# Performance work log

Hardware: AMD Instinct MI355X
Metric: run time of the kernel (lower is better)

The kernel has to match this reference:

```python
import jax, jax.numpy as jnp
import numpy as np

B, S, N, HID = 4, 512, 128, 64


def setup_inputs() -> dict:
    key = jax.random.key(0)
    ks = jax.random.split(key, 32)
    def rn(k, shape, scale=0.1):
        return jax.random.normal(k, shape, dtype=jnp.float32) * scale
    adj = jax.random.randint(ks[0], (N, N), 0, 2).astype(jnp.int32)
    adj = adj.at[jnp.arange(N), jnp.arange(N)].set(1)  # self loops
    inp = {
        'x': jax.random.normal(ks[1], (B, S, N, 1), dtype=jnp.float32),
        'adj': adj,
        'emb_w': rn(ks[2], (1, 16)), 'emb_b': jnp.zeros((16,), jnp.float32),
        'gat1_W': rn(ks[3], (16, 16)), 'gat1_a': rn(ks[4], (32, 1)),
        'gat2_W': rn(ks[5], (16, 8)), 'gat2_a': rn(ks[6], (16, 1)),
        'Wih0': rn(ks[7], (4 * HID, N)), 'Whh0': rn(ks[8], (4 * HID, HID)),
        'bih0': jnp.zeros((4 * HID,), jnp.float32), 'bhh0': jnp.zeros((4 * HID,), jnp.float32),
        'Wih1': rn(ks[9], (4 * HID, HID)), 'Whh1': rn(ks[10], (4 * HID, HID)),
        'bih1': jnp.zeros((4 * HID,), jnp.float32), 'bhh1': jnp.zeros((4 * HID,), jnp.float32),
    }
    comb = HID + 8 * N
    for i, name in enumerate(['dir', 'ret', 'vol']):
        o = 2 if name == 'vol' else 1
        inp[name + '_w1'] = rn(ks[11 + 4 * i], (comb, 32))
        inp[name + '_b1'] = jnp.zeros((32,), jnp.float32)
        inp[name + '_w2'] = rn(ks[12 + 4 * i], (32, o))
        inp[name + '_b2'] = jnp.zeros((o,), jnp.float32)
    return inp


def _gat(h, W, a, mask):
    # e_ij = leakyrelu(a1 . Wh_i + a2 . Wh_j): avoid torch's [M,N,N,2F] concat.
    Wh = h @ W                                  # [M, N, F]
    Fo = W.shape[1]
    f1 = Wh @ a[:Fo]                            # [M, N, 1]
    f2 = Wh @ a[Fo:]                            # [M, N, 1]
    e = jax.nn.leaky_relu(f1 + jnp.swapaxes(f2, 1, 2), 0.2)  # [M, N, N]
    e = jnp.where(mask, e, jnp.float32(-9e15))
    attn = jax.nn.softmax(e, axis=2)
    return attn @ Wh                            # [M, N, F]


def _lstm_layer(xs, Wih, Whh, bih, bhh):
    # xs: [S, B, I]; PyTorch gate order i, f, g, o
    Bsz = xs.shape[1]
    Hd = Whh.shape[1]
    def step(carry, xt):
        h, c = carry
        g = xt @ Wih.T + h @ Whh.T + bih + bhh
        i, f, gg, o = jnp.split(g, 4, axis=-1)
        c = jax.nn.sigmoid(f) * c + jax.nn.sigmoid(i) * jnp.tanh(gg)
        h = jax.nn.sigmoid(o) * jnp.tanh(c)
        return (h, c), h
    init = (jnp.zeros((Bsz, Hd), xs.dtype), jnp.zeros((Bsz, Hd), xs.dtype))
    _, hs = jax.lax.scan(step, init, xs)
    return hs


def reference(x, adj, emb_w, emb_b, gat1_W, gat1_a, gat2_W, gat2_a,
              Wih0, Whh0, bih0, bhh0, Wih1, Whh1, bih1, bhh1,
              dir_w1, dir_b1, dir_w2, dir_b2,
              ret_w1, ret_b1, ret_w2, ret_b2,
              vol_w1, vol_b1, vol_w2, vol_b2):
    Bz, Sz, Nz, _ = x.shape
    mask = (adj > 0)[None]                      # [1, N, N], broadcast over B*S
    xe = (x @ emb_w + emb_b).reshape(Bz * Sz, Nz, 16)
    xg = jax.nn.elu(_gat(xe, gat1_W, gat1_a, mask))   # gat1 concat=True -> elu
    xg = _gat(xg, gat2_W, gat2_a, mask)               # gat2 concat=False
    xg_out = xg.reshape(Bz, Sz, Nz * 8)[:, -1, :]
    xs = jnp.swapaxes(x.reshape(Bz, Sz, Nz), 0, 1)    # [S, B, N]
    hs = _lstm_layer(xs, Wih0, Whh0, bih0, bhh0)
    hs = _lstm_layer(hs, Wih1, Whh1, bih1, bhh1)      # inter-layer dropout off (eval)
    xl_out = hs[-1]                                   # [B, 64]
    c = jnp.concatenate([xl_out, xg_out], axis=1)     # [B, 64 + 8N]
    def head(w1, b1, w2, b2):
        return jax.nn.relu(c @ w1 + b1) @ w2 + b2
    return (head(dir_w1, dir_b1, dir_w2, dir_b2),
            head(ret_w1, ret_b1, ret_w2, ret_b2),
            head(vol_w1, vol_b1, vol_w2, vol_b2))
```

## Files before the change

kernel.cpp:

```cpp
#include <hip/hip_runtime.h>

#define SEQ   512
#define BATCH 4
#define NN    128
#define HID   64
#define G4    256
#define MAGIC 0x13579BDF

typedef _Float16 half2v __attribute__((ext_vector_type(2)));

__device__ __forceinline__ float frcp(float x)  { return __builtin_amdgcn_rcpf(x); }
__device__ __forceinline__ float fsigm(float x) { return frcp(1.f + __expf(-x)); }
__device__ __forceinline__ float ftanh(float x) { return 1.f - 2.f * frcp(1.f + __expf(2.f * x)); }
__device__ __forceinline__ float lrelu(float x) { return x > 0.f ? x : 0.2f * x; }
__device__ __forceinline__ float dot4f(float4 w, float4 h) {
  return fmaf(w.x, h.x, fmaf(w.y, h.y, fmaf(w.z, h.z, w.w * h.w)));
}
__device__ __forceinline__ void pin4(float4& v) {
  asm volatile("" : "+v"(v.x), "+v"(v.y), "+v"(v.z), "+v"(v.w));
}
__device__ __forceinline__ float qsum(float x) {
  x += __int_as_float(__builtin_amdgcn_update_dpp(
      0, __float_as_int(x), 0xB1, 0xF, 0xF, true));
  x += __int_as_float(__builtin_amdgcn_update_dpp(
      0, __float_as_int(x), 0x4E, 0xF, 0xF, true));
  return x;
}
__device__ __forceinline__ half2v u2h(unsigned u) {
  return __builtin_bit_cast(half2v, u);
}
__device__ __forceinline__ half2v pk16(float lo, float hi) {
  return __builtin_bit_cast(half2v, __builtin_amdgcn_cvt_pkrtz(lo, hi));
}
__device__ __forceinline__ float fdot2(half2v a, half2v b, float c) {
#if __has_builtin(__builtin_amdgcn_fdot2)
  return __builtin_amdgcn_fdot2(a, b, c, false);
#else
  float d = c;
  asm("v_dot2_f32_f16 %0, %1, %2, %0" : "+v"(d) : "v"(a), "v"(b));
  return d;
#endif
}
__device__ __forceinline__ float dot8h(const half2v* w, const uint4& a,
                                       const uint4& b, float acc) {
  acc = fdot2(w[0], u2h(a.x), acc);
  acc = fdot2(w[1], u2h(a.y), acc);
  acc = fdot2(w[2], u2h(a.z), acc);
  acc = fdot2(w[3], u2h(a.w), acc);
  acc = fdot2(w[4], u2h(b.x), acc);
  acc = fdot2(w[5], u2h(b.y), acc);
  acc = fdot2(w[6], u2h(b.z), acc);
  acc = fdot2(w[7], u2h(b.w), acc);
  return acc;
}

#define BAR_LDS() asm volatile("s_waitcnt lgkmcnt(0)\n\ts_barrier" ::: "memory")

__global__ __attribute__((amdgpu_flat_work_group_size(256, 256),
                          amdgpu_waves_per_eu(1, 4)))
void fused_all(
    const float* __restrict__ x, const int* __restrict__ adj,
    const float* __restrict__ emb_w, const float* __restrict__ emb_b,
    const float* __restrict__ W1, const float* __restrict__ a1,
    const float* __restrict__ W2, const float* __restrict__ a2,
    const float* __restrict__ Wih0, const float* __restrict__ Whh0,
    const float* __restrict__ bih0, const float* __restrict__ bhh0,
    const float* __restrict__ Wih1, const float* __restrict__ Whh1,
    const float* __restrict__ bih1, const float* __restrict__ bhh1,
    const float* __restrict__ dw1, const float* __restrict__ db1,
    const float* __restrict__ dw2, const float* __restrict__ db2,
    const float* __restrict__ rw1, const float* __restrict__ rb1,
    const float* __restrict__ rw2, const float* __restrict__ rb2,
    const float* __restrict__ vw1, const float* __restrict__ vb1,
    const float* __restrict__ vw2, const float* __restrict__ vb2,
    float* __restrict__ X0T, float* __restrict__ xg,
    int* __restrict__ flags, float* __restrict__ out)
{
  const int bid = blockIdx.x;
  const int tid = threadIdx.x;

  if (bid >= 4) {
    const int c = bid - 4;
    __shared__ __align__(16) float xls[NN];
    {
      const int g = tid;
      float4 w4[32];
      {
        const float4* wp = reinterpret_cast<const float4*>(Wih0 + g * NN);
#pragma unroll
        for (int i = 0; i < 32; ++i) w4[i] = wp[i];
#pragma unroll
        for (int i = 0; i < 32; ++i) pin4(w4[i]);
      }
      const float bsum = bih0[g] + bhh0[g];
      for (int phase = 0; phase < 4; ++phase) {
        const int T = c + 128 * phase;
        for (int bb = 0; bb < BATCH; ++bb) {
          if (tid < NN) xls[tid] = x[(bb * SEQ + T) * NN + tid];
          __syncthreads();
          {
            const float4* hp = reinterpret_cast<const float4*>(xls);
            float p0 = 0.f, p1 = 0.f, p2 = 0.f, p3 = 0.f;
#pragma unroll
            for (int k = 0; k < 32; k += 4) {
              p0 += dot4f(w4[k],     hp[k]);
              p1 += dot4f(w4[k + 1], hp[k + 1]);
              p2 += dot4f(w4[k + 2], hp[k + 2]);
              p3 += dot4f(w4[k + 3], hp[k + 3]);
            }
            X0T[(4 * T + bb) * G4 + (g & 63) * 4 + (g >> 6)] =
                ((p0 + p1) + (p2 + p3)) + bsum;
          }
          __syncthreads();
        }
        if (tid == 0 && phase == 0)
          __hip_atomic_store(&flags[c], MAGIC, __ATOMIC_RELEASE,
                             __HIP_MEMORY_SCOPE_AGENT);
        if (tid == 0 && phase == 3)
          __hip_atomic_store(&flags[128 + c], MAGIC, __ATOMIC_RELEASE,
                             __HIP_MEMORY_SCOPE_AGENT);
      }
    }
    if (bid >= 8) return;

    const int b = bid - 4;
    __shared__ float adjm[NN * 129];
    __shared__ __align__(16) float gxls[NN];
    __shared__ float u[16], v[16];
    __shared__ float Wh2[NN][9];
    __shared__ float f1b[NN], f2b[NN];
    __shared__ float p[NN];

    for (int idx = tid; idx < NN * NN; idx += 256)
      adjm[(idx >> 7) * 129 + (idx & 127)] = (adj[idx] > 0) ? 1.f : 0.f;
    if (tid < NN) gxls[tid] = x[(b * SEQ + (SEQ - 1)) * NN + tid];
    if (tid < 16) {
      float uu = 0.f, vv = 0.f;
      for (int fp = 0; fp < 16; ++fp) {
        uu += emb_w[fp] * W1[fp * 16 + tid];
        vv += emb_b[fp] * W1[fp * 16 + tid];
      }
      u[tid] = uu; v[tid] = vv;
    }
    __syncthreads();
    float s1 = 0.f, t1 = 0.f, s2 = 0.f, t2 = 0.f;
    for (int f = 0; f < 16; ++f) {
      s1 += u[f] * a1[f];      t1 += v[f] * a1[f];
      s2 += u[f] * a1[16 + f]; t2 += v[f] * a1[16 + f];
    }
    if (tid < NN) {
      const int i = tid;
      const float f1i = gxls[i] * s1 + t1;
      float m = -1e30f;
      for (int j = 0; j < NN; ++j)
        if (adjm[i * 129 + j] != 0.f)
          m = fmaxf(m, lrelu(f1i + gxls[j] * s2 + t2));
      float ssum = 0.f, ps = 0.f;
      for (int j = 0; j < NN; ++j)
        if (adjm[i * 129 + j] != 0.f) {
          const float wgt = __expf(lrelu(f1i + gxls[j] * s2 + t2) - m);
          ssum += wgt; ps += wgt * gxls[j];
        }
      p[i] = ps / ssum;
    }
    __syncthreads();
    if (tid < NN) {
      const int i = tid;
      float xg1[16];
#pragma unroll
      for (int f = 0; f < 16; ++f) {
        const float ov = p[i] * u[f] + v[f];
        xg1[f] = ov > 0.f ? ov : expm1f(ov);
      }
      float wrow[8];
#pragma unroll
      for (int f2 = 0; f2 < 8; ++f2) wrow[f2] = 0.f;
#pragma unroll
      for (int f = 0; f < 16; ++f) {
        const float xv = xg1[f];
#pragma unroll
        for (int f2 = 0; f2 < 8; ++f2) wrow[f2] += xv * W2[f * 8 + f2];
      }
      float fb1 = 0.f, fb2 = 0.f;
#pragma unroll
      for (int f2 = 0; f2 < 8; ++f2) {
        Wh2[i][f2] = wrow[f2];
        fb1 += wrow[f2] * a2[f2];
        fb2 += wrow[f2] * a2[8 + f2];
      }
      f1b[i] = fb1; f2b[i] = fb2;
    }
    __syncthreads();
    if (tid < NN) {
      const int i = tid;
      const float fi = f1b[i];
      float m = -1e30f;
      for (int j = 0; j < NN; ++j)
        if (adjm[i * 129 + j] != 0.f)
          m = fmaxf(m, lrelu(fi + f2b[j]));
      float ssum = 0.f;
      float o[8];
#pragma unroll
      for (int f2 = 0; f2 < 8; ++f2) o[f2] = 0.f;
      for (int j = 0; j < NN; ++j)
        if (adjm[i * 129 + j] != 0.f) {
          const float wgt = __expf(lrelu(fi + f2b[j]) - m);
          ssum += wgt;
#pragma unroll
          for (int f2 = 0; f2 < 8; ++f2) o[f2] += wgt * Wh2[j][f2];
        }
      const float inv = 1.f / ssum;
#pragma unroll
      for (int f2 = 0; f2 < 8; ++f2)
        xg[b * (NN * 8) + i * 8 + f2] = o[f2] * inv;
    }
    __syncthreads();
    if (tid == 0)
      __hip_atomic_store(&flags[256 + b], MAGIC, __ATOMIC_RELEASE,
                         __HIP_MEMORY_SCOPE_AGENT);
    return;
  }

  const int b   = bid;
  const int t   = tid;
  const int uu  = t >> 2, q2 = t & 3;
  const int r   = t;

  __shared__ __align__(16) half2v hb16[2][2][HID / 2];
  __shared__ float cbuf[1088];
  __shared__ float hidc[96];

  half2v wA[4][8], wB[4][8], wC[4][8];
#pragma unroll
  for (int j = 0; j < 4; ++j) {
    const int row = (uu + 64 * j) * HID + 16 * q2;
    const float* wa = Whh0 + row;
    const float* wb = Wih1 + row;
    const float* wc = Whh1 + row;
#pragma unroll
    for (int c = 0; c < 4; ++c) {
      const float4 va = *reinterpret_cast<const float4*>(wa + 4 * c);
      const float4 vb = *reinterpret_cast<const float4*>(wb + 4 * c);
      const float4 vc = *reinterpret_cast<const float4*>(wc + 4 * c);
      wA[j][2 * c]     = half2v{(_Float16)va.x, (_Float16)va.y};
      wA[j][2 * c + 1] = half2v{(_Float16)va.z, (_Float16)va.w};
      wB[j][2 * c]     = half2v{(_Float16)vb.x, (_Float16)vb.y};
      wB[j][2 * c + 1] = half2v{(_Float16)vb.z, (_Float16)vb.w};
      wC[j][2 * c]     = half2v{(_Float16)vc.x, (_Float16)vc.y};
      wC[j][2 * c + 1] = half2v{(_Float16)vc.z, (_Float16)vc.w};
    }
  }
  float4 b1v;
  b1v.x = bih1[uu]       + bhh1[uu];
  b1v.y = bih1[uu + 64]  + bhh1[uu + 64];
  b1v.z = bih1[uu + 128] + bhh1[uu + 128];
  b1v.w = bih1[uu + 192] + bhh1[uu + 192];

  if (t < 128) reinterpret_cast<unsigned*>(hb16)[t] = 0u;
  float cst0 = 0.f, cst1 = 0.f;
  const float* X0b = X0T + b * G4 + uu * 4;

  int c_ok;
  {
    if (t < 32) {
      while (__hip_atomic_fetch_add(&flags[t], 0, __ATOMIC_ACQUIRE,
                                    __HIP_MEMORY_SCOPE_AGENT) != MAGIC) {}
    }
    __syncthreads();
    c_ok = 31;
  }

  const uint4* h0A = reinterpret_cast<const uint4*>(&hb16[0][0][0]) + 2 * q2;
  const uint4* h0B = reinterpret_cast<const uint4*>(&hb16[1][0][0]) + 2 * q2;
  const uint4* h1A = reinterpret_cast<const uint4*>(&hb16[0][1][0]) + 2 * q2;
  const uint4* h1B = reinterpret_cast<const uint4*>(&hb16[1][1][0]) + 2 * q2;

  float4 xa0 = *reinterpret_cast<const float4*>(X0b + 0 * (BATCH * G4));
  float4 xa1 = *reinterpret_cast<const float4*>(X0b + 1 * (BATCH * G4));
  float4 xa2 = *reinterpret_cast<const float4*>(X0b + 2 * (BATCH * G4));
  float4 xa3 = *reinterpret_cast<const float4*>(X0b + 3 * (BATCH * G4));

#define PACK_WRITE(LAYER, WB, HV)                                              \
  do {                                                                         \
    const float pr_ = __int_as_float(__builtin_amdgcn_update_dpp(              \
        0, __float_as_int(HV), 0x141, 0xF, 0xF, true));                        \
    if ((r & 7) == 0)                                                          \
      hb16[WB][LAYER][r >> 3] = pk16((HV), pr_);                               \
  } while (0)

#define LSTM_STEP(TT, RB, WB, XV)                                              \
  do {                                                                         \
    const uint4* h0p = (RB) ? h0B : h0A;                                       \
    const uint4* h1p = (RB) ? h1B : h1A;                                       \
    const uint4 ha = h0p[0], hbb = h0p[1];                                     \
    const uint4 ga = h1p[0], gbb = h1p[1];                                     \
    float A0 = dot8h(wA[0], ha, hbb, 0.f);                                     \
    float A1 = dot8h(wA[1], ha, hbb, 0.f);                                     \
    float A2 = dot8h(wA[2], ha, hbb, 0.f);                                     \
    float A3 = dot8h(wA[3], ha, hbb, 0.f);                                     \
    float B0 = dot8h(wB[0], ha, hbb, 0.f);                                     \
    float B1 = dot8h(wB[1], ha, hbb, 0.f);                                     \
    float B2 = dot8h(wB[2], ha, hbb, 0.f);                                     \
    float B3 = dot8h(wB[3], ha, hbb, 0.f);                                     \
    float C0 = dot8h(wC[0], ga, gbb, 0.f);                                     \
    float C1 = dot8h(wC[1], ga, gbb, 0.f);                                     \
    float C2 = dot8h(wC[2], ga, gbb, 0.f);                                     \
    float C3 = dot8h(wC[3], ga, gbb, 0.f);                                     \
    const float SA0 = qsum(A0), SA1 = qsum(A1), SA2 = qsum(A2), SA3 = qsum(A3);\
    if ((TT) < SEQ) {                                                          \
      const float gi = fsigm(SA0 + (XV).x);                                    \
      const float gf = fsigm(SA1 + (XV).y);                                    \
      const float gg = ftanh(SA2 + (XV).z);                                    \
      const float go = fsigm(SA3 + (XV).w);                                    \
      cst0 = fmaf(gf, cst0, gi * gg);                                          \
      const float hv = go * ftanh(cst0);                                       \
      PACK_WRITE(0, WB, hv);                                                   \
    }                                                                          \
    const float SB0 = qsum(B0), SB1 = qsum(B1), SB2 = qsum(B2), SB3 = qsum(B3);\
    const float SC0 = qsum(C0), SC1 = qsum(C1), SC2 = qsum(C2), SC3 = qsum(C3);\
    if ((TT) >= 1) {                                                           \
      const float gi = fsigm(SC0 + SB0 + b1v.x);                               \
      const float gf = fsigm(SC1 + SB1 + b1v.y);                               \
      const float gg = ftanh(SC2 + SB2 + b1v.z);                               \
      const float go = fsigm(SC3 + SB3 + b1v.w);                               \
      cst1 = fmaf(gf, cst1, gi * gg);                                          \
      const float hv = go * ftanh(cst1);                                       \
      PACK_WRITE(1, WB, hv);                                                   \
    }                                                                          \
    BAR_LDS();                                                                 \
  } while (0)

  for (int tt = 0; tt < SEQ; tt += 4) {
    if (tt + 36 > c_ok && c_ok < 255) {
      const int base = c_ok + 1;
      if (t < 32 && base + t <= 255) {
        while (__hip_atomic_fetch_add(&flags[base + t], 0, __ATOMIC_ACQUIRE,
                                      __HIP_MEMORY_SCOPE_AGENT) != MAGIC) {}
      }
      __syncthreads();
      c_ok = (base + 31 < 255) ? base + 31 : 255;
    }
#pragma unroll
    for (int j = 0; j < 4; ++j) {
      asm volatile("" : "+v"(wA[j][0]), "+v"(wA[j][1]), "+v"(wA[j][2]),
                        "+v"(wA[j][3]), "+v"(wA[j][4]), "+v"(wA[j][5]),
                        "+v"(wA[j][6]), "+v"(wA[j][7]));
      asm volatile("" : "+v"(wB[j][0]), "+v"(wB[j][1]), "+v"(wB[j][2]),
                        "+v"(wB[j][3]), "+v"(wB[j][4]), "+v"(wB[j][5]),
                        "+v"(wB[j][6]), "+v"(wB[j][7]));
      asm volatile("" : "+v"(wC[j][0]), "+v"(wC[j][1]), "+v"(wC[j][2]),
                        "+v"(wC[j][3]), "+v"(wC[j][4]), "+v"(wC[j][5]),
                        "+v"(wC[j][6]), "+v"(wC[j][7]));
    }
    float4 xb0 = xa0, xb1 = xa1, xb2 = xa2, xb3 = xa3;
    if (tt + 4 < SEQ) {
      xb0 = *reinterpret_cast<const float4*>(X0b + (tt + 4) * (BATCH * G4));
      xb1 = *reinterpret_cast<const float4*>(X0b + (tt + 5) * (BATCH * G4));
      xb2 = *reinterpret_cast<const float4*>(X0b + (tt + 6) * (BATCH * G4));
      xb3 = *reinterpret_cast<const float4*>(X0b + (tt + 7) * (BATCH * G4));
    }
    LSTM_STEP(tt + 0, 0, 1, xa0);
    LSTM_STEP(tt + 1, 1, 0, xa1);
    LSTM_STEP(tt + 2, 0, 1, xa2);
    LSTM_STEP(tt + 3, 1, 0, xa3);
    xa0 = xb0; xa1 = xb1; xa2 = xb2; xa3 = xb3;
  }
  LSTM_STEP(512, 0, 1, xa0);
#undef LSTM_STEP
#undef PACK_WRITE

  if (t == 0) {
    while (__hip_atomic_fetch_add(&flags[256 + b], 0, __ATOMIC_ACQUIRE,
                                  __HIP_MEMORY_SCOPE_AGENT) != MAGIC) {}
  }
  __syncthreads();

  if (t < 64) {
    const _Float16* hh = reinterpret_cast<const _Float16*>(&hb16[1][1][0]);
    cbuf[t] = (float)hh[t];
  }
  for (int k = t; k < 1024; k += 256) cbuf[64 + k] = xg[b * 1024 + k];
  __syncthreads();
  if (t < 96) {
    const int head = t >> 5, h = t & 31;
    const float* w1 = (head == 0) ? dw1 : (head == 1) ? rw1 : vw1;
    const float* b1 = (head == 0) ? db1 : (head == 1) ? rb1 : vb1;
    float a0 = 0.f, a1v = 0.f, a2v = 0.f, a3v = 0.f;
    for (int k = 0; k < 1088; k += 4) {
      a0  = fmaf(cbuf[k],     w1[k * 32 + h],       a0);
      a1v = fmaf(cbuf[k + 1], w1[(k + 1) * 32 + h], a1v);
      a2v = fmaf(cbuf[k + 2], w1[(k + 2) * 32 + h], a2v);
      a3v = fmaf(cbuf[k + 3], w1[(k + 3) * 32 + h], a3v);
    }
    hidc[head * 32 + h] = fmaxf(b1[h] + ((a0 + a1v) + (a2v + a3v)), 0.f);
  }
  __syncthreads();
  if (t < 4) {
    const int head2 = (t < 2) ? t : 2;
    const int o = (t < 2) ? 0 : (t - 2);
    const int odim = (t < 2) ? 1 : 2;
    const float* w2  = (head2 == 0) ? dw2 : (head2 == 1) ? rw2 : vw2;
    const float* b2p = (head2 == 0) ? db2 : (head2 == 1) ? rb2 : vb2;
    float acc = b2p[o];
    for (int hh = 0; hh < 32; ++hh)
      acc = fmaf(hidc[head2 * 32 + hh], w2[hh * odim + o], acc);
    const int off = (t == 0) ? b : (t == 1) ? (4 + b) : (8 + 2 * b + o);
    out[off] = acc;
  }
}

extern "C" void kernel_launch(void* const* d_in, const int* in_sizes, int n_in,
                              void* d_out, int out_size, void* d_ws, size_t ws_size,
                              hipStream_t stream) {
  const float* x     = (const float*)d_in[0];
  const int*   adj   = (const int*)  d_in[1];
  const float* emb_w = (const float*)d_in[2];
  const float* emb_b = (const float*)d_in[3];
  const float* g1W   = (const float*)d_in[4];
  const float* g1a   = (const float*)d_in[5];
  const float* g2W   = (const float*)d_in[6];
  const float* g2a   = (const float*)d_in[7];
  const float* Wih0  = (const float*)d_in[8];
  const float* Whh0  = (const float*)d_in[9];
  const float* bih0  = (const float*)d_in[10];
  const float* bhh0  = (const float*)d_in[11];
  const float* Wih1  = (const float*)d_in[12];
  const float* Whh1  = (const float*)d_in[13];
  const float* bih1  = (const float*)d_in[14];
  const float* bhh1  = (const float*)d_in[15];
  const float* dw1 = (const float*)d_in[16]; const float* db1 = (const float*)d_in[17];
  const float* dw2 = (const float*)d_in[18]; const float* db2 = (const float*)d_in[19];
  const float* rw1 = (const float*)d_in[20]; const float* rb1 = (const float*)d_in[21];
  const float* rw2 = (const float*)d_in[22]; const float* rb2 = (const float*)d_in[23];
  const float* vw1 = (const float*)d_in[24]; const float* vb1 = (const float*)d_in[25];
  const float* vw2 = (const float*)d_in[26]; const float* vb2 = (const float*)d_in[27];

  float* ws = (float*)d_ws;
  float* X0 = ws;
  float* xg = ws + SEQ * BATCH * G4;
  int*  flg = (int*)(xg + BATCH * NN * 8);
  float* out = (float*)d_out;

  hipLaunchKernelGGL(fused_all, dim3(132), dim3(256), 0, stream,
                     x, adj, emb_w, emb_b, g1W, g1a, g2W, g2a,
                     Wih0, Whh0, bih0, bhh0, Wih1, Whh1, bih1, bhh1,
                     dw1, db1, dw2, db2, rw1, rb1, rw2, rb2,
                     vw1, vb1, vw2, vb2,
                     X0, xg, flg, out);
}
```

Baseline: 412.8 us.

## Specialize LSTM waves per matrix with a three-stage wavefront pipeline

Restructures the recurrent LSTM loop so that each of three waves owns one weight matrix (Whh0, Wih1, Whh1) in full, 64 fp16 elements per row per lane. This removes the 4-lane DPP reductions and the redundant per-lane splitting of rows. Layer 1's input projection is passed through a shared-memory buffer and consumed one step later, which turns the two layers into a three-stage skewed pipeline. The fourth wave sits idle, each step still ends in a block barrier, and per-lane register pressure rises to 128 weight registers.

```diff
diff --git a/kernel.cpp b/kernel.cpp
--- a/kernel.cpp
+++ b/kernel.cpp
@@ -18,13 +18,6 @@
 }
 __device__ __forceinline__ void pin4(float4& v) {
   asm volatile("" : "+v"(v.x), "+v"(v.y), "+v"(v.z), "+v"(v.w));
-}
-__device__ __forceinline__ float qsum(float x) {
-  x += __int_as_float(__builtin_amdgcn_update_dpp(
-      0, __float_as_int(x), 0xB1, 0xF, 0xF, true));
-  x += __int_as_float(__builtin_amdgcn_update_dpp(
-      0, __float_as_int(x), 0x4E, 0xF, 0xF, true));
-  return x;
 }
 __device__ __forceinline__ half2v u2h(unsigned u) {
   return __builtin_bit_cast(half2v, u);
@@ -52,6 +45,10 @@
   acc = fdot2(w[6], u2h(b.z), acc);
   acc = fdot2(w[7], u2h(b.w), acc);
   return acc;
+}
+__device__ __forceinline__ float nbr1(float x) {
+  return __int_as_float(__builtin_amdgcn_update_dpp(
+      0, __float_as_int(x), 0xB1, 0xF, 0xF, true));
 }
 
 #define BAR_LDS() asm volatile("s_waitcnt lgkmcnt(0)\n\ts_barrier" ::: "memory")
@@ -223,42 +220,41 @@
 
   const int b   = bid;
   const int t   = tid;
-  const int uu  = t >> 2, q2 = t & 3;
-  const int r   = t;
-
-  __shared__ __align__(16) half2v hb16[2][2][HID / 2];
+  const int wid = t >> 6;
+  const int l   = t & 63;
+
+  __shared__ __align__(16) unsigned hb0[2][32];
+  __shared__ __align__(16) unsigned hb1[2][32];
+  __shared__ __align__(16) float SBb[2][G4];
   __shared__ float cbuf[1088];
   __shared__ float hidc[96];
 
-  half2v wA[4][8], wB[4][8], wC[4][8];
-#pragma unroll
-  for (int j = 0; j < 4; ++j) {
-    const int row = (uu + 64 * j) * HID + 16 * q2;
-    const float* wa = Whh0 + row;
-    const float* wb = Wih1 + row;
-    const float* wc = Whh1 + row;
-#pragma unroll
-    for (int c = 0; c < 4; ++c) {
-      const float4 va = *reinterpret_cast<const float4*>(wa + 4 * c);
-      const float4 vb = *reinterpret_cast<const float4*>(wb + 4 * c);
-      const float4 vc = *reinterpret_cast<const float4*>(wc + 4 * c);
-      wA[j][2 * c]     = half2v{(_Float16)va.x, (_Float16)va.y};
-      wA[j][2 * c + 1] = half2v{(_Float16)va.z, (_Float16)va.w};
-      wB[j][2 * c]     = half2v{(_Float16)vb.x, (_Float16)vb.y};
-      wB[j][2 * c + 1] = half2v{(_Float16)vb.z, (_Float16)vb.w};
-      wC[j][2 * c]     = half2v{(_Float16)vc.x, (_Float16)vc.y};
-      wC[j][2 * c + 1] = half2v{(_Float16)vc.z, (_Float16)vc.w};
-    }
-  }
-  float4 b1v;
-  b1v.x = bih1[uu]       + bhh1[uu];
-  b1v.y = bih1[uu + 64]  + bhh1[uu + 64];
-  b1v.z = bih1[uu + 128] + bhh1[uu + 128];
-  b1v.w = bih1[uu + 192] + bhh1[uu + 192];
-
-  if (t < 128) reinterpret_cast<unsigned*>(hb16)[t] = 0u;
+  const float* Wsrc = (wid == 0) ? Whh0 : (wid == 1) ? Wih1 : Whh1;
+  half2v w[4][32];
+  if (wid < 3) {
+#pragma unroll
+    for (int j = 0; j < 4; ++j) {
+      const float* wr = Wsrc + (l + 64 * j) * HID;
+#pragma unroll
+      for (int c = 0; c < 16; ++c) {
+        const float4 wv = *reinterpret_cast<const float4*>(wr + 4 * c);
+        w[j][2 * c]     = half2v{(_Float16)wv.x, (_Float16)wv.y};
+        w[j][2 * c + 1] = half2v{(_Float16)wv.z, (_Float16)wv.w};
+      }
+    }
+  }
+  float4 b1v = make_float4(0.f, 0.f, 0.f, 0.f);
+  if (wid == 1) {
+    b1v.x = bih1[l]       + bhh1[l];
+    b1v.y = bih1[l + 64]  + bhh1[l + 64];
+    b1v.z = bih1[l + 128] + bhh1[l + 128];
+    b1v.w = bih1[l + 192] + bhh1[l + 192];
+  }
+
+  if (t < 64) reinterpret_cast<unsigned*>(hb0)[t] = 0u;
+  if (t < 64) reinterpret_cast<unsigned*>(hb1)[t] = 0u;
   float cst0 = 0.f, cst1 = 0.f;
-  const float* X0b = X0T + b * G4 + uu * 4;
+  const float* X0b = X0T + b * G4 + l * 4;
 
   int c_ok;
   {
@@ -270,68 +266,79 @@
     c_ok = 31;
   }
 
-  const uint4* h0A = reinterpret_cast<const uint4*>(&hb16[0][0][0]) + 2 * q2;
-  const uint4* h0B = reinterpret_cast<const uint4*>(&hb16[1][0][0]) + 2 * q2;
-  const uint4* h1A = reinterpret_cast<const uint4*>(&hb16[0][1][0]) + 2 * q2;
-  const uint4* h1B = reinterpret_cast<const uint4*>(&hb16[1][1][0]) + 2 * q2;
-
-  float4 xa0 = *reinterpret_cast<const float4*>(X0b + 0 * (BATCH * G4));
-  float4 xa1 = *reinterpret_cast<const float4*>(X0b + 1 * (BATCH * G4));
-  float4 xa2 = *reinterpret_cast<const float4*>(X0b + 2 * (BATCH * G4));
-  float4 xa3 = *reinterpret_cast<const float4*>(X0b + 3 * (BATCH * G4));
-
-#define PACK_WRITE(LAYER, WB, HV)                                              \
+  float4 xa0 = make_float4(0.f, 0.f, 0.f, 0.f), xa1 = xa0;
+  if (wid == 0) {
+    xa0 = *reinterpret_cast<const float4*>(X0b + 0 * (BATCH * G4));
+    xa1 = *reinterpret_cast<const float4*>(X0b + 1 * (BATCH * G4));
+  }
+
+#define LOAD_H8(SRC, RB)                                                       \
+  const uint4* hp_ = reinterpret_cast<const uint4*>(&SRC[RB][0]);              \
+  const uint4 v0 = hp_[0], v1 = hp_[1], v2 = hp_[2], v3 = hp_[3];              \
+  const uint4 v4 = hp_[4], v5 = hp_[5], v6 = hp_[6], v7 = hp_[7]
+
+#define DOT64(G, ACC0)                                                         \
+  dot8h(&w[G][24], v6, v7,                                                     \
+  dot8h(&w[G][16], v4, v5,                                                     \
+  dot8h(&w[G][8],  v2, v3,                                                     \
+  dot8h(&w[G][0],  v0, v1, (ACC0)))))
+
+#define PACK_W(DST, WB, HV)                                                    \
   do {                                                                         \
-    const float pr_ = __int_as_float(__builtin_amdgcn_update_dpp(              \
-        0, __float_as_int(HV), 0x141, 0xF, 0xF, true));                        \
-    if ((r & 7) == 0)                                                          \
-      hb16[WB][LAYER][r >> 3] = pk16((HV), pr_);                               \
+    const float nb_ = nbr1(HV);                                                \
+    if ((l & 1) == 0)                                                          \
+      DST[WB][l >> 1] = __builtin_bit_cast(unsigned, pk16((HV), nb_));         \
   } while (0)
 
-#define LSTM_STEP(TT, RB, WB, XV)                                              \
+#define INT_STEP(K, RB, WB, XV)                                                \
   do {                                                                         \
-    const uint4* h0p = (RB) ? h0B : h0A;                                       \
-    const uint4* h1p = (RB) ? h1B : h1A;                                       \
-    const uint4 ha = h0p[0], hbb = h0p[1];                                     \
-    const uint4 ga = h1p[0], gbb = h1p[1];                                     \
-    float A0 = dot8h(wA[0], ha, hbb, 0.f);                                     \
-    float A1 = dot8h(wA[1], ha, hbb, 0.f);                                     \
-    float A2 = dot8h(wA[2], ha, hbb, 0.f);                                     \
-    float A3 = dot8h(wA[3], ha, hbb, 0.f);                                     \
-    float B0 = dot8h(wB[0], ha, hbb, 0.f);                                     \
-    float B1 = dot8h(wB[1], ha, hbb, 0.f);                                     \
-    float B2 = dot8h(wB[2], ha, hbb, 0.f);                                     \
-    float B3 = dot8h(wB[3], ha, hbb, 0.f);                                     \
-    float C0 = dot8h(wC[0], ga, gbb, 0.f);                                     \
-    float C1 = dot8h(wC[1], ga, gbb, 0.f);                                     \
-    float C2 = dot8h(wC[2], ga, gbb, 0.f);                                     \
-    float C3 = dot8h(wC[3], ga, gbb, 0.f);                                     \
-    const float SA0 = qsum(A0), SA1 = qsum(A1), SA2 = qsum(A2), SA3 = qsum(A3);\
-    if ((TT) < SEQ) {                                                          \
-      const float gi = fsigm(SA0 + (XV).x);                                    \
-      const float gf = fsigm(SA1 + (XV).y);                                    \
-      const float gg = ftanh(SA2 + (XV).z);                                    \
-      const float go = fsigm(SA3 + (XV).w);                                    \
-      cst0 = fmaf(gf, cst0, gi * gg);                                          \
-      const float hv = go * ftanh(cst0);                                       \
-      PACK_WRITE(0, WB, hv);                                                   \
-    }                                                                          \
-    const float SB0 = qsum(B0), SB1 = qsum(B1), SB2 = qsum(B2), SB3 = qsum(B3);\
-    const float SC0 = qsum(C0), SC1 = qsum(C1), SC2 = qsum(C2), SC3 = qsum(C3);\
-    if ((TT) >= 1) {                                                           \
-      const float gi = fsigm(SC0 + SB0 + b1v.x);                               \
-      const float gf = fsigm(SC1 + SB1 + b1v.y);                               \
-      const float gg = ftanh(SC2 + SB2 + b1v.z);                               \
-      const float go = fsigm(SC3 + SB3 + b1v.w);                               \
-      cst1 = fmaf(gf, cst1, gi * gg);                                          \
-      const float hv = go * ftanh(cst1);                                       \
-      PACK_WRITE(1, WB, hv);                                                   \
+    if (wid == 0) {                                                            \
+      if ((K) < SEQ) {                                                         \
+        LOAD_H8(hb0, RB);                                                      \
+        const float A0 = DOT64(0, 0.f);                                        \
+        const float A1 = DOT64(1, 0.f);                                        \
+        const float A2 = DOT64(2, 0.f);                                        \
+        const float A3 = DOT64(3, 0.f);                                        \
+        const float gi = fsigm(A0 + (XV).x);                                   \
+        const float gf = fsigm(A1 + (XV).y);                                   \
+        const float gg = ftanh(A2 + (XV).z);                                   \
+        const float go = fsigm(A3 + (XV).w);                                   \
+        cst0 = fmaf(gf, cst0, gi * gg);                                        \
+        const float hv = go * ftanh(cst0);                                     \
+        PACK_W(hb0, WB, hv);                                                   \
+      }                                                                        \
+    } else if (wid == 1) {                                                     \
+      if ((K) >= 1 && (K) <= SEQ) {                                            \
+        LOAD_H8(hb0, RB);                                                      \
+        const float B0 = DOT64(0, b1v.x);                                      \
+        const float B1 = DOT64(1, b1v.y);                                      \
+        const float B2 = DOT64(2, b1v.z);                                      \
+        const float B3 = DOT64(3, b1v.w);                                      \
+        *reinterpret_cast<float4*>(&SBb[WB][l * 4]) =                          \
+            make_float4(B0, B1, B2, B3);                                       \
+      }                                                                        \
+    } else if (wid == 2) {                                                     \
+      if ((K) >= 2) {                                                          \
+        LOAD_H8(hb1, RB);                                                      \
+        const float C0 = DOT64(0, 0.f);                                        \
+        const float C1 = DOT64(1, 0.f);                                        \
+        const float C2 = DOT64(2, 0.f);                                        \
+        const float C3 = DOT64(3, 0.f);                                        \
+        const float4 sb = *reinterpret_cast<const float4*>(&SBb[RB][l * 4]);   \
+        const float gi = fsigm(C0 + sb.x);                                     \
+        const float gf = fsigm(C1 + sb.y);                                     \
+        const float gg = ftanh(C2 + sb.z);                                     \
+        const float go = fsigm(C3 + sb.w);                                     \
+        cst1 = fmaf(gf, cst1, gi * gg);                                        \
+        const float hv = go * ftanh(cst1);                                     \
+        PACK_W(hb1, WB, hv);                                                   \
+      }                                                                        \
     }                                                                          \
     BAR_LDS();                                                                 \
   } while (0)
 
-  for (int tt = 0; tt < SEQ; tt += 4) {
-    if (tt + 36 > c_ok && c_ok < 255) {
+  for (int k = 0; k < SEQ + 2; k += 2) {
+    if (k + 8 > c_ok && c_ok < 255) {
       const int base = c_ok + 1;
       if (t < 32 && base + t <= 255) {
         while (__hip_atomic_fetch_add(&flags[base + t], 0, __ATOMIC_ACQUIRE,
@@ -340,34 +347,33 @@
       __syncthreads();
       c_ok = (base + 31 < 255) ? base + 31 : 255;
     }
-#pragma unroll
-    for (int j = 0; j < 4; ++j) {
-      asm volatile("" : "+v"(wA[j][0]), "+v"(wA[j][1]), "+v"(wA[j][2]),
-                        "+v"(wA[j][3]), "+v"(wA[j][4]), "+v"(wA[j][5]),
-                        "+v"(wA[j][6]), "+v"(wA[j][7]));
-      asm volatile("" : "+v"(wB[j][0]), "+v"(wB[j][1]), "+v"(wB[j][2]),
-                        "+v"(wB[j][3]), "+v"(wB[j][4]), "+v"(wB[j][5]),
-                        "+v"(wB[j][6]), "+v"(wB[j][7]));
-      asm volatile("" : "+v"(wC[j][0]), "+v"(wC[j][1]), "+v"(wC[j][2]),
-                        "+v"(wC[j][3]), "+v"(wC[j][4]), "+v"(wC[j][5]),
-                        "+v"(wC[j][6]), "+v"(wC[j][7]));
-    }
-    float4 xb0 = xa0, xb1 = xa1, xb2 = xa2, xb3 = xa3;
-    if (tt + 4 < SEQ) {
-      xb0 = *reinterpret_cast<const float4*>(X0b + (tt + 4) * (BATCH * G4));
-      xb1 = *reinterpret_cast<const float4*>(X0b + (tt + 5) * (BATCH * G4));
-      xb2 = *reinterpret_cast<const float4*>(X0b + (tt + 6) * (BATCH * G4));
-      xb3 = *reinterpret_cast<const float4*>(X0b + (tt + 7) * (BATCH * G4));
-    }
-    LSTM_STEP(tt + 0, 0, 1, xa0);
-    LSTM_STEP(tt + 1, 1, 0, xa1);
-    LSTM_STEP(tt + 2, 0, 1, xa2);
-    LSTM_STEP(tt + 3, 1, 0, xa3);
-    xa0 = xb0; xa1 = xb1; xa2 = xb2; xa3 = xb3;
-  }
-  LSTM_STEP(512, 0, 1, xa0);
-#undef LSTM_STEP
-#undef PACK_WRITE
+    if (wid < 3) {
+#pragma unroll
+      for (int j = 0; j < 4; ++j) {
+        half2v* wp = &w[j][0];
+        asm volatile("" : "+v"(wp[0]), "+v"(wp[1]), "+v"(wp[2]), "+v"(wp[3]),
+                          "+v"(wp[4]), "+v"(wp[5]), "+v"(wp[6]), "+v"(wp[7]));
+        asm volatile("" : "+v"(wp[8]), "+v"(wp[9]), "+v"(wp[10]), "+v"(wp[11]),
+                          "+v"(wp[12]), "+v"(wp[13]), "+v"(wp[14]), "+v"(wp[15]));
+        asm volatile("" : "+v"(wp[16]), "+v"(wp[17]), "+v"(wp[18]), "+v"(wp[19]),
+                          "+v"(wp[20]), "+v"(wp[21]), "+v"(wp[22]), "+v"(wp[23]));
+        asm volatile("" : "+v"(wp[24]), "+v"(wp[25]), "+v"(wp[26]), "+v"(wp[27]),
+                          "+v"(wp[28]), "+v"(wp[29]), "+v"(wp[30]), "+v"(wp[31]));
+      }
+    }
+    float4 xb0 = xa0, xb1 = xa1;
+    if (wid == 0 && k + 2 < SEQ) {
+      xb0 = *reinterpret_cast<const float4*>(X0b + (k + 2) * (BATCH * G4));
+      xb1 = *reinterpret_cast<const float4*>(X0b + (k + 3) * (BATCH * G4));
+    }
+    INT_STEP(k,     1, 0, xa0);
+    INT_STEP(k + 1, 0, 1, xa1);
+    xa0 = xb0; xa1 = xb1;
+  }
+#undef INT_STEP
+#undef PACK_W
+#undef DOT64
+#undef LOAD_H8
 
   if (t == 0) {
     while (__hip_atomic_fetch_add(&flags[256 + b], 0, __ATOMIC_ACQUIRE,
@@ -376,7 +382,7 @@
   __syncthreads();
 
   if (t < 64) {
-    const _Float16* hh = reinterpret_cast<const _Float16*>(&hb16[1][1][0]);
+    const _Float16* hh = reinterpret_cast<const _Float16*>(&hb1[1][0]);
     cbuf[t] = (float)hh[t];
   }
   for (int k = t; k < 1024; k += 256) cbuf[64 + k] = xg[b * 1024 + k];
```

Result: faster. 400.6 us (-3.0%).
